# Optimization experiments

Hardware: AMD Instinct MI355X
Metric: run time of the kernel (lower is better)

## Reference

```python
import jax, jax.numpy as jnp
import numpy as np
import math

N_EMBD = 2048
N_HEAD = 16
HEAD_DIM = N_EMBD // N_HEAD  # 128
K = 8
P = 2
B = 1
T = 2048
EPS = 1e-6


def _rms_norm(x):
    return x * jax.lax.rsqrt(jnp.mean(x * x, axis=-1, keepdims=True) + EPS)


def _rope(x, cos, sin):
    # x: [B, T, H, D]; cos/sin: [T, D//2]
    d = x.shape[-1] // 2
    x1, x2 = x[..., :d], x[..., d:]
    c = cos[None, :, None, :]
    s = sin[None, :, None, :]
    return jnp.concatenate([x1 * c + x2 * s, -x1 * s + x2 * c], axis=-1)


def setup_inputs() -> dict:
    key = jax.random.key(0)
    ks = jax.random.split(key, 8)
    x = jax.random.normal(ks[0], (B, T, N_EMBD), jnp.float32)
    half = HEAD_DIM // 2
    inv_freq = 1.0 / (10000.0 ** (np.arange(half, dtype=np.float32) / half))
    ang = np.arange(T, dtype=np.float32)[:, None] * inv_freq[None, :]
    cos = jnp.asarray(np.cos(ang), jnp.float32)
    sin = jnp.asarray(np.sin(ang), jnp.float32)
    sc = 1.0 / math.sqrt(N_EMBD)
    Wq = jax.random.normal(ks[1], (N_EMBD, N_EMBD), jnp.float32) * sc
    Wk = jax.random.normal(ks[2], (N_EMBD, N_EMBD), jnp.float32) * sc
    Wv = jax.random.normal(ks[3], (N_EMBD, N_EMBD), jnp.float32) * sc
    Wproj = jax.random.normal(ks[4], (N_EMBD, N_EMBD), jnp.float32) * sc
    scd = 1.0 / math.sqrt(HEAD_DIM)
    Wdq = jax.random.normal(ks[5], (K, HEAD_DIM), jnp.float32) * scd
    Wdk = jax.random.normal(ks[6], (K, HEAD_DIM), jnp.float32) * scd
    return {"x": x, "cos": cos, "sin": sin, "Wq": Wq, "Wk": Wk, "Wv": Wv, "Wproj": Wproj, "Wdq": Wdq, "Wdk": Wdk}


def reference(x, cos, sin, Wq, Wk, Wv, Wproj, Wdq, Wdk):
    Bq, Tq, C = x.shape
    q = (x @ Wq.T).reshape(Bq, Tq, N_HEAD, HEAD_DIM)
    k = (x @ Wk.T).reshape(Bq, Tq, N_HEAD, HEAD_DIM)
    v = (x @ Wv.T).reshape(Bq, Tq, N_HEAD, HEAD_DIM)
    q = _rms_norm(_rope(q, cos, sin))
    k = _rms_norm(_rope(k, cos, sin))
    q = jnp.swapaxes(q, 1, 2)  # [B,H,T,D]
    k = jnp.swapaxes(k, 1, 2)
    v = jnp.swapaxes(v, 1, 2)
    # base-p digits in {0..p-1}; p=2 -> bits
    qd = jnp.floor(jax.nn.sigmoid(jnp.einsum('bhtd,kd->bhtk', q, Wdq)) * (P - 0.01)).astype(jnp.int32)
    kd = jnp.floor(jax.nn.sigmoid(jnp.einsum('bhtd,kd->bhtk', k, Wdk)) * (P - 0.01)).astype(jnp.int32)
    # lcp >= K-1  <=>  first K-1 digits all equal; pack them into one code
    pw = (P ** jnp.arange(K - 1)).astype(jnp.int32)  # [K-1]
    qc = jnp.sum(qd[..., : K - 1] * pw, axis=-1)  # [B,H,T]
    kc = jnp.sum(kd[..., : K - 1] * pw, axis=-1)
    lcp_mask = qc[..., :, None] == kc[..., None, :]  # [B,H,Tq,Tk]
    causal = jnp.tril(jnp.ones((Tq, Tq), dtype=bool))
    mask = lcp_mask & causal
    scores = jnp.einsum('bhqd,bhkd->bhqk', q, k) * (1.0 / math.sqrt(HEAD_DIM))
    s = jnp.where(mask, scores, -1e30)
    w = jax.nn.softmax(s, axis=-1)
    w = jnp.where(mask, w, 0.0)
    any_valid = jnp.any(mask, axis=-1, keepdims=True)
    w = jnp.where(any_valid, w, 0.0)  # fully-masked rows -> zero output (torch gives NaN)
    y = jnp.einsum('bhqk,bhkd->bhqd', w, v)
    y = jnp.swapaxes(y, 1, 2).reshape(Bq, Tq, C)
    return y @ Wproj.T
```

## Files before the change

kernel.cpp:

```cpp
#include <hip/hip_runtime.h>
#include <hip/hip_bf16.h>
#include <math.h>

#define T 2048
#define C 2048
#define NH 16
#define HD 128
#define SCALE 0.08838834764831845f
#define WL_CAP 2048
#define MARG 1e-4f

typedef short s16x8 __attribute__((ext_vector_type(8)));
typedef float f32x4 __attribute__((ext_vector_type(4)));
typedef _Float16 f16;
typedef f16 f16x8 __attribute__((ext_vector_type(8)));

__device__ __forceinline__ float wave_sum(float v) {
  #pragma unroll
  for (int o = 32; o > 0; o >>= 1) v += __shfl_xor(v, o, 64);
  return v;
}
__device__ __forceinline__ unsigned short f2bf(float f) {
  unsigned u = __float_as_uint(f);
  u += 0x7FFFu + ((u >> 16) & 1u);
  return (unsigned short)(u >> 16);
}

__global__ __launch_bounds__(256) void to_bf16(const float* __restrict__ in,
                                               unsigned short* __restrict__ outp,
                                               int n4) {
  int i = blockIdx.x * blockDim.x + threadIdx.x;
  const int stride = gridDim.x * blockDim.x;
  for (; i < n4; i += stride) {
    float4 v = ((const float4*)in)[i];
    ushort4 o;
    o.x = f2bf(v.x); o.y = f2bf(v.y); o.z = f2bf(v.z); o.w = f2bf(v.w);
    ((ushort4*)outp)[i] = o;
  }
}

#define PRESC 4096.0f
#define S0F 5.9604644775390625e-8f
#define S1F 2.9103830456733704e-11f
#define S2F 1.4210854715202004e-14f

__device__ __forceinline__ void split4(float4 v, ushort4& hi, ushort4& lo) {
  float s0 = v.x * PRESC, s1 = v.y * PRESC, s2 = v.z * PRESC, s3 = v.w * PRESC;
  union { f16 h[4]; ushort4 u; } H, L;
  H.h[0] = (f16)s0; H.h[1] = (f16)s1; H.h[2] = (f16)s2; H.h[3] = (f16)s3;
  L.h[0] = (f16)((s0 - (float)H.h[0]) * 2048.0f);
  L.h[1] = (f16)((s1 - (float)H.h[1]) * 2048.0f);
  L.h[2] = (f16)((s2 - (float)H.h[2]) * 2048.0f);
  L.h[3] = (f16)((s3 - (float)H.h[3]) * 2048.0f);
  hi = H.u; lo = L.u;
}

__global__ __launch_bounds__(256) void split_f16(const float* __restrict__ in,
                                                 unsigned short* __restrict__ hip_,
                                                 unsigned short* __restrict__ lop,
                                                 int n4) {
  int i = blockIdx.x * blockDim.x + threadIdx.x;
  const int stride = gridDim.x * blockDim.x;
  for (; i < n4; i += stride) {
    ushort4 h, l;
    split4(((const float4*)in)[i], h, l);
    ((ushort4*)hip_)[i] = h;
    ((ushort4*)lop)[i] = l;
  }
}

__global__ __launch_bounds__(256) void pre_split3(const float* __restrict__ x,
                                                  const float* __restrict__ Wq,
                                                  const float* __restrict__ Wk,
                                                  unsigned short* __restrict__ xh,
                                                  unsigned short* __restrict__ xl,
                                                  unsigned short* __restrict__ wqh,
                                                  unsigned short* __restrict__ wql,
                                                  unsigned short* __restrict__ wkh,
                                                  unsigned short* __restrict__ wkl,
                                                  int n4) {
  const float* __restrict__ in;
  unsigned short *oh, *ol;
  if (blockIdx.y == 0)      { in = x;  oh = xh;  ol = xl;  }
  else if (blockIdx.y == 1) { in = Wq; oh = wqh; ol = wql; }
  else                      { in = Wk; oh = wkh; ol = wkl; }
  int i = blockIdx.x * blockDim.x + threadIdx.x;
  const int stride = gridDim.x * blockDim.x;
  for (; i < n4; i += stride) {
    ushort4 h, l;
    split4(((const float4*)in)[i], h, l);
    ((ushort4*)oh)[i] = h;
    ((ushort4*)ol)[i] = l;
  }
}

__global__ __launch_bounds__(256) void to_f16h(const float* __restrict__ in,
                                               unsigned short* __restrict__ outp,
                                               int n4) {
  int i = blockIdx.x * blockDim.x + threadIdx.x;
  const int stride = gridDim.x * blockDim.x;
  for (; i < n4; i += stride) {
    float4 v = ((const float4*)in)[i];
    union { f16 h[4]; ushort4 u; } H;
    H.h[0] = (f16)(v.x * PRESC); H.h[1] = (f16)(v.y * PRESC);
    H.h[2] = (f16)(v.z * PRESC); H.h[3] = (f16)(v.w * PRESC);
    ((ushort4*)outp)[i] = H.u;
  }
}

__global__ __launch_bounds__(256) void post_h2(const float* __restrict__ Y,
                                               const float* __restrict__ Wproj,
                                               unsigned short* __restrict__ yh,
                                               unsigned short* __restrict__ wph,
                                               int n4) {
  const float* __restrict__ in = blockIdx.y ? Wproj : Y;
  unsigned short* __restrict__ outp = blockIdx.y ? wph : yh;
  int i = blockIdx.x * blockDim.x + threadIdx.x;
  const int stride = gridDim.x * blockDim.x;
  for (; i < n4; i += stride) {
    float4 v = ((const float4*)in)[i];
    union { f16 h[4]; ushort4 u; } H;
    H.h[0] = (f16)(v.x * PRESC); H.h[1] = (f16)(v.y * PRESC);
    H.h[2] = (f16)(v.z * PRESC); H.h[3] = (f16)(v.w * PRESC);
    ((ushort4*)outp)[i] = H.u;
  }
}

#define SBM 64
#define SBN 128
#define SBK 32

__global__ __launch_bounds__(256, 2) void gemm_qkf(const unsigned short* __restrict__ xhp,
                                                   const unsigned short* __restrict__ xlp,
                                                   const unsigned short* __restrict__ wqh,
                                                   const unsigned short* __restrict__ wql,
                                                   const unsigned short* __restrict__ wkh,
                                                   const unsigned short* __restrict__ wkl,
                                                   float* __restrict__ Qo,
                                                   float* __restrict__ Ko) {
  __shared__ unsigned short Ah[2][128 * 32];
  __shared__ unsigned short Av[2][128 * 32];
  __shared__ unsigned short Bh[2][128 * 32];
  __shared__ unsigned short Bv[2][128 * 32];
  const int tid = threadIdx.x;
  const int bm = blockIdx.x * 128;
  const int bn = blockIdx.y * 64;
  const int wv = tid >> 6, lane = tid & 63;
  const int wm = wv & 1, wn = wv >> 1;
  const int lrow = lane & 15, lquad = lane >> 4;

  const int sr = tid >> 2, qg = tid & 3;
  const int qs = qg ^ ((sr >> 1) & 3);

  f32x4 acc0[4][4], acc1[4][4];
  #pragma unroll
  for (int i = 0; i < 4; ++i)
    #pragma unroll
    for (int j = 0; j < 4; ++j) {
      acc0[i][j] = (f32x4){0.f, 0.f, 0.f, 0.f};
      acc1[i][j] = (f32x4){0.f, 0.f, 0.f, 0.f};
    }

  {
    uint4 a0H = *(const uint4*)(xhp + (size_t)(bm + sr) * C + qg * 8);
    uint4 a0L = *(const uint4*)(xlp + (size_t)(bm + sr) * C + qg * 8);
    uint4 a1H = *(const uint4*)(xhp + (size_t)(bm + 64 + sr) * C + qg * 8);
    uint4 a1L = *(const uint4*)(xlp + (size_t)(bm + 64 + sr) * C + qg * 8);
    uint4 bqH = *(const uint4*)(wqh + (size_t)(bn + sr) * C + qg * 8);
    uint4 bqL = *(const uint4*)(wql + (size_t)(bn + sr) * C + qg * 8);
    uint4 bkH = *(const uint4*)(wkh + (size_t)(bn + sr) * C + qg * 8);
    uint4 bkL = *(const uint4*)(wkl + (size_t)(bn + sr) * C + qg * 8);
    *(uint4*)&Ah[0][sr * 32 + qs * 8] = a0H;
    *(uint4*)&Av[0][sr * 32 + qs * 8] = a0L;
    *(uint4*)&Ah[0][(64 + sr) * 32 + qs * 8] = a1H;
    *(uint4*)&Av[0][(64 + sr) * 32 + qs * 8] = a1L;
    *(uint4*)&Bh[0][sr * 32 + qs * 8] = bqH;
    *(uint4*)&Bv[0][sr * 32 + qs * 8] = bqL;
    *(uint4*)&Bh[0][(64 + sr) * 32 + qs * 8] = bkH;
    *(uint4*)&Bv[0][(64 + sr) * 32 + qs * 8] = bkL;
  }
  __syncthreads();

  const int niter = C / 32;
  for (int it = 0; it < niter; ++it) {
    const int cur = it & 1;
    const bool has = (it + 1) < niter;
    uint4 a0H, a0L, a1H, a1L, bqH, bqL, bkH, bkL;
    if (has) {
      const int k0 = (it + 1) * 32;
      a0H = *(const uint4*)(xhp + (size_t)(bm + sr) * C + k0 + qg * 8);
      a0L = *(const uint4*)(xlp + (size_t)(bm + sr) * C + k0 + qg * 8);
      a1H = *(const uint4*)(xhp + (size_t)(bm + 64 + sr) * C + k0 + qg * 8);
      a1L = *(const uint4*)(xlp + (size_t)(bm + 64 + sr) * C + k0 + qg * 8);
      bqH = *(const uint4*)(wqh + (size_t)(bn + sr) * C + k0 + qg * 8);
      bqL = *(const uint4*)(wql + (size_t)(bn + sr) * C + k0 + qg * 8);
      bkH = *(const uint4*)(wkh + (size_t)(bn + sr) * C + k0 + qg * 8);
      bkL = *(const uint4*)(wkl + (size_t)(bn + sr) * C + k0 + qg * 8);
    }
    f16x8 ah[4], av[4], bh[4], bv[4];
    #pragma unroll
    for (int mi = 0; mi < 4; ++mi) {
      const int r = wm * 64 + mi * 16 + lrow;
      const int q = lquad ^ ((r >> 1) & 3);
      ah[mi] = *(const f16x8*)&Ah[cur][r * 32 + q * 8];
      av[mi] = *(const f16x8*)&Av[cur][r * 32 + q * 8];
    }
    #pragma unroll
    for (int ni = 0; ni < 4; ++ni) {
      const int r = wn * 64 + ni * 16 + lrow;
      const int q = lquad ^ ((r >> 1) & 3);
      bh[ni] = *(const f16x8*)&Bh[cur][r * 32 + q * 8];
      bv[ni] = *(const f16x8*)&Bv[cur][r * 32 + q * 8];
    }
    #pragma unroll
    for (int mi = 0; mi < 4; ++mi)
      #pragma unroll
      for (int ni = 0; ni < 4; ++ni) {
        acc0[mi][ni] = __builtin_amdgcn_mfma_f32_16x16x32_f16(ah[mi], bh[ni], acc0[mi][ni], 0, 0, 0);
        acc1[mi][ni] = __builtin_amdgcn_mfma_f32_16x16x32_f16(ah[mi], bv[ni], acc1[mi][ni], 0, 0, 0);
        acc1[mi][ni] = __builtin_amdgcn_mfma_f32_16x16x32_f16(av[mi], bh[ni], acc1[mi][ni], 0, 0, 0);
      }
    if (has) {
      const int nxt = cur ^ 1;
      *(uint4*)&Ah[nxt][sr * 32 + qs * 8] = a0H;
      *(uint4*)&Av[nxt][sr * 32 + qs * 8] = a0L;
      *(uint4*)&Ah[nxt][(64 + sr) * 32 + qs * 8] = a1H;
      *(uint4*)&Av[nxt][(64 + sr) * 32 + qs * 8] = a1L;
      *(uint4*)&Bh[nxt][sr * 32 + qs * 8] = bqH;
      *(uint4*)&Bv[nxt][sr * 32 + qs * 8] = bqL;
      *(uint4*)&Bh[nxt][(64 + sr) * 32 + qs * 8] = bkH;
      *(uint4*)&Bv[nxt][(64 + sr) * 32 + qs * 8] = bkL;
    }
    __syncthreads();
  }
  float* __restrict__ Cc = wn ? Ko : Qo;
  #pragma unroll
  for (int mi = 0; mi < 4; ++mi)
    #pragma unroll
    for (int ni = 0; ni < 4; ++ni)
      #pragma unroll
      for (int r = 0; r < 4; ++r) {
        int row = bm + wm * 64 + mi * 16 + lquad * 4 + r;
        int col = bn + ni * 16 + lrow;
        Cc[(size_t)row * C + col] = acc0[mi][ni][r] * S0F + acc1[mi][ni][r] * S1F;
      }
}

__global__ __launch_bounds__(256) void gemm_h1(const unsigned short* __restrict__ A,
                                               const unsigned short* __restrict__ B,
                                               float* __restrict__ Cc) {
  __shared__ unsigned short Ah[2][SBM * SBK];
  __shared__ unsigned short Bh[2][SBN * SBK];
  const int tid = threadIdx.x;
  const int bm = blockIdx.x * SBM;
  const int bn = blockIdx.y * SBN;
  const int wv = tid >> 6, lane = tid & 63;
  const int wm = wv & 1, wn = wv >> 1;
  const int lrow = lane & 15, lquad = lane >> 4;

  const int a_row = tid >> 2, qg = tid & 3;
  const int a_qs = qg ^ ((a_row >> 1) & 3);
  const int b_row0 = tid >> 2;
  const int b_qs = qg ^ ((b_row0 >> 1) & 3);

  f32x4 acc[2][4];
  #pragma unroll
  for (int i = 0; i < 2; ++i)
    #pragma unroll
    for (int j = 0; j < 4; ++j) acc[i][j] = (f32x4){0.f, 0.f, 0.f, 0.f};

  {
    uint4 av = *(const uint4*)(A + (size_t)(bm + a_row) * C + qg * 8);
    uint4 b0 = *(const uint4*)(B + (size_t)(bn + b_row0) * C + qg * 8);
    uint4 b1 = *(const uint4*)(B + (size_t)(bn + 64 + b_row0) * C + qg * 8);
    *(uint4*)&Ah[0][a_row * SBK + a_qs * 8] = av;
    *(uint4*)&Bh[0][b_row0 * SBK + b_qs * 8] = b0;
    *(uint4*)&Bh[0][(64 + b_row0) * SBK + b_qs * 8] = b1;
  }
  __syncthreads();

  const int niter = C / SBK;
  for (int it = 0; it < niter; ++it) {
    const int cur = it & 1;
    const bool has = (it + 1) < niter;
    uint4 avn, b0n, b1n;
    if (has) {
      const int k0 = (it + 1) * SBK;
      avn = *(const uint4*)(A + (size_t)(bm + a_row) * C + k0 + qg * 8);
      b0n = *(const uint4*)(B + (size_t)(bn + b_row0) * C + k0 + qg * 8);
      b1n = *(const uint4*)(B + (size_t)(bn + 64 + b_row0) * C + k0 + qg * 8);
    }
    f16x8 af[2], bfr[4];
    #pragma unroll
    for (int mi = 0; mi < 2; ++mi) {
      const int r = wm * 32 + mi * 16 + lrow;
      const int q = lquad ^ ((r >> 1) & 3);
      af[mi] = *(const f16x8*)&Ah[cur][r * SBK + q * 8];
    }
    #pragma unroll
    for (int ni = 0; ni < 4; ++ni) {
      const int r = wn * 64 + ni * 16 + lrow;
      const int q = lquad ^ ((r >> 1) & 3);
      bfr[ni] = *(const f16x8*)&Bh[cur][r * SBK + q * 8];
    }
    #pragma unroll
    for (int mi = 0; mi < 2; ++mi)
      #pragma unroll
      for (int ni = 0; ni < 4; ++ni)
        acc[mi][ni] = __builtin_amdgcn_mfma_f32_16x16x32_f16(af[mi], bfr[ni], acc[mi][ni], 0, 0, 0);
    if (has) {
      const int nxt = cur ^ 1;
      *(uint4*)&Ah[nxt][a_row * SBK + a_qs * 8] = avn;
      *(uint4*)&Bh[nxt][b_row0 * SBK + b_qs * 8] = b0n;
      *(uint4*)&Bh[nxt][(64 + b_row0) * SBK + b_qs * 8] = b1n;
    }
    __syncthreads();
  }
  #pragma unroll
  for (int mi = 0; mi < 2; ++mi)
    #pragma unroll
    for (int ni = 0; ni < 4; ++ni)
      #pragma unroll
      for (int r = 0; r < 4; ++r) {
        int row = bm + wm * 32 + mi * 16 + lquad * 4 + r;
        int col = bn + wn * 64 + ni * 16 + lrow;
        Cc[(size_t)row * C + col] = acc[mi][ni][r] * S0F;
      }
}

__device__ __forceinline__ void split8(const float4 v0, const float4 v1,
                                       uint4& hi, uint4& lo) {
  float s[8] = {v0.x * PRESC, v0.y * PRESC, v0.z * PRESC, v0.w * PRESC,
                v1.x * PRESC, v1.y * PRESC, v1.z * PRESC, v1.w * PRESC};
  union { uint4 u; f16 h[8]; } H, L;
  #pragma unroll
  for (int i = 0; i < 8; ++i) {
    f16 h2 = (f16)s[i];
    float d = s[i] - (float)h2;
    H.h[i] = h2;
    L.h[i] = (f16)(d * 2048.0f);
  }
  hi = H.u; lo = L.u;
}

__global__ __launch_bounds__(256, 2) void gemm_qk_split16(const float* __restrict__ A,
                                                          const float* __restrict__ Wq,
                                                          const float* __restrict__ Wk,
                                                          float* __restrict__ Qo,
                                                          float* __restrict__ Ko) {
  const float* __restrict__ Bw = blockIdx.z ? Wk : Wq;
  float* __restrict__ Cc = blockIdx.z ? Ko : Qo;
  __shared__ unsigned short Ah[2][SBM * SBK];
  __shared__ unsigned short Av[2][SBM * SBK];
  __shared__ unsigned short Bh[2][SBN * SBK];
  __shared__ unsigned short Bv[2][SBN * SBK];
  const int tid = threadIdx.x;
  const int bm = blockIdx.x * SBM;
  const int bn = blockIdx.y * SBN;
  const int wv = tid >> 6, lane = tid & 63;
  const int wm = wv & 1, wn = wv >> 1;
  const int lrow = lane & 15, lquad = lane >> 4;

  const int a_row = tid >> 2, qg = tid & 3;
  const int a_qs = qg ^ ((a_row >> 1) & 3);
  const int b_row0 = tid >> 2;
  const int b_qs = qg ^ ((b_row0 >> 1) & 3);

  f32x4 acc[3][2][4];
  #pragma unroll
  for (int g = 0; g < 3; ++g)
    #pragma unroll
    for (int i = 0; i < 2; ++i)
      #pragma unroll
      for (int j = 0; j < 4; ++j) acc[g][i][j] = (f32x4){0.f, 0.f, 0.f, 0.f};

  {
    const float* pA  = A  + (size_t)(bm + a_row) * C + qg * 8;
    const float* pB0 = Bw + (size_t)(bn + b_row0) * C + qg * 8;
    const float* pB1 = Bw + (size_t)(bn + 64 + b_row0) * C + qg * 8;
    uint4 h, l;
    split8(*(const float4*)pA, *(const float4*)(pA + 4), h, l);
    *(uint4*)&Ah[0][a_row * SBK + a_qs * 8] = h;
    *(uint4*)&Av[0][a_row * SBK + a_qs * 8] = l;
    split8(*(const float4*)pB0, *(const float4*)(pB0 + 4), h, l);
    *(uint4*)&Bh[0][b_row0 * SBK + b_qs * 8] = h;
    *(uint4*)&Bv[0][b_row0 * SBK + b_qs * 8] = l;
    split8(*(const float4*)pB1, *(const float4*)(pB1 + 4), h, l);
    *(uint4*)&Bh[0][(64 + b_row0) * SBK + b_qs * 8] = h;
    *(uint4*)&Bv[0][(64 + b_row0) * SBK + b_qs * 8] = l;
  }
  __syncthreads();

  const int niter = C / SBK;
  for (int it = 0; it < niter; ++it) {
    const int cur = it & 1;
    const bool has = (it + 1) < niter;
    float4 a0n, a1n, b00n, b01n, b10n, b11n;
    if (has) {
      const int k0 = (it + 1) * SBK;
      const float* pA  = A  + (size_t)(bm + a_row) * C + k0 + qg * 8;
      const float* pB0 = Bw + (size_t)(bn + b_row0) * C + k0 + qg * 8;
      const float* pB1 = Bw + (size_t)(bn + 64 + b_row0) * C + k0 + qg * 8;
      a0n = *(const float4*)pA;   a1n = *(const float4*)(pA + 4);
      b00n = *(const float4*)pB0; b01n = *(const float4*)(pB0 + 4);
      b10n = *(const float4*)pB1; b11n = *(const float4*)(pB1 + 4);
    }
    f16x8 ah[2], av[2], bh[4], bv[4];
    #pragma unroll
    for (int mi = 0; mi < 2; ++mi) {
      const int r = wm * 32 + mi * 16 + lrow;
      const int q = lquad ^ ((r >> 1) & 3);
      ah[mi] = *(const f16x8*)&Ah[cur][r * SBK + q * 8];
      av[mi] = *(const f16x8*)&Av[cur][r * SBK + q * 8];
    }
    #pragma unroll
    for (int ni = 0; ni < 4; ++ni) {
      const int r = wn * 64 + ni * 16 + lrow;
      const int q = lquad ^ ((r >> 1) & 3);
      bh[ni] = *(const f16x8*)&Bh[cur][r * SBK + q * 8];
      bv[ni] = *(const f16x8*)&Bv[cur][r * SBK + q * 8];
    }
    #pragma unroll
    for (int mi = 0; mi < 2; ++mi)
      #pragma unroll
      for (int ni = 0; ni < 4; ++ni) {
        acc[0][mi][ni] = __builtin_amdgcn_mfma_f32_16x16x32_f16(ah[mi], bh[ni], acc[0][mi][ni], 0, 0, 0);
        acc[1][mi][ni] = __builtin_amdgcn_mfma_f32_16x16x32_f16(ah[mi], bv[ni], acc[1][mi][ni], 0, 0, 0);
        acc[1][mi][ni] = __builtin_amdgcn_mfma_f32_16x16x32_f16(av[mi], bh[ni], acc[1][mi][ni], 0, 0, 0);
        acc[2][mi][ni] = __builtin_amdgcn_mfma_f32_16x16x32_f16(av[mi], bv[ni], acc[2][mi][ni], 0, 0, 0);
      }
    if (has) {
      const int nxt = cur ^ 1;
      uint4 h, l;
      split8(a0n, a1n, h, l);
      *(uint4*)&Ah[nxt][a_row * SBK + a_qs * 8] = h;
      *(uint4*)&Av[nxt][a_row * SBK + a_qs * 8] = l;
      split8(b00n, b01n, h, l);
      *(uint4*)&Bh[nxt][b_row0 * SBK + b_qs * 8] = h;
      *(uint4*)&Bv[nxt][b_row0 * SBK + b_qs * 8] = l;
      split8(b10n, b11n, h, l);
      *(uint4*)&Bh[nxt][(64 + b_row0) * SBK + b_qs * 8] = h;
      *(uint4*)&Bv[nxt][(64 + b_row0) * SBK + b_qs * 8] = l;
    }
    __syncthreads();
  }
  #pragma unroll
  for (int mi = 0; mi < 2; ++mi)
    #pragma unroll
    for (int ni = 0; ni < 4; ++ni)
      #pragma unroll
      for (int r = 0; r < 4; ++r) {
        int row = bm + wm * 32 + mi * 16 + lquad * 4 + r;
        int col = bn + wn * 64 + ni * 16 + lrow;
        float v = acc[0][mi][ni][r] * S0F + (acc[1][mi][ni][r] * S1F + acc[2][mi][ni][r] * S2F);
        Cc[(size_t)row * C + col] = v;
      }
}

#define VBM 64
#define VBN 128
#define VBK 32

__global__ __launch_bounds__(256) void gemm_bf16n(const unsigned short* __restrict__ A,
                                                  const unsigned short* __restrict__ B,
                                                  float* __restrict__ Cc) {
  __shared__ unsigned short Al[2][VBM * VBK];
  __shared__ unsigned short Bl[2][VBN * VBK];
  const int tid = threadIdx.x;
  const int bm = blockIdx.x * VBM;
  const int bn = blockIdx.y * VBN;
  const int wv = tid >> 6, lane = tid & 63;
  const int wm = wv & 1, wn = wv >> 1;
  const int lrow = lane & 15, lquad = lane >> 4;

  const int a_row = tid >> 2, qg = tid & 3;
  const int a_qs = qg ^ ((a_row >> 1) & 3);
  const int b_row0 = tid >> 2;
  const int b_qs = qg ^ ((b_row0 >> 1) & 3);

  f32x4 acc[2][4];
  #pragma unroll
  for (int i = 0; i < 2; ++i)
    #pragma unroll
    for (int j = 0; j < 4; ++j) acc[i][j] = (f32x4){0.f, 0.f, 0.f, 0.f};

  {
    uint4 av = *(const uint4*)(A + (size_t)(bm + a_row) * C + qg * 8);
    uint4 b0 = *(const uint4*)(B + (size_t)(bn + b_row0) * C + qg * 8);
    uint4 b1 = *(const uint4*)(B + (size_t)(bn + 64 + b_row0) * C + qg * 8);
    *(uint4*)&Al[0][a_row * VBK + a_qs * 8] = av;
    *(uint4*)&Bl[0][b_row0 * VBK + b_qs * 8] = b0;
    *(uint4*)&Bl[0][(64 + b_row0) * VBK + b_qs * 8] = b1;
  }
  __syncthreads();

  const int niter = C / VBK;
  for (int it = 0; it < niter; ++it) {
    const int cur = it & 1;
    const bool has = (it + 1) < niter;
    uint4 avn, b0n, b1n;
    if (has) {
      const int k0 = (it + 1) * VBK;
      avn = *(const uint4*)(A + (size_t)(bm + a_row) * C + k0 + qg * 8);
      b0n = *(const uint4*)(B + (size_t)(bn + b_row0) * C + k0 + qg * 8);
      b1n = *(const uint4*)(B + (size_t)(bn + 64 + b_row0) * C + k0 + qg * 8);
    }
    s16x8 af[2], bfr[4];
    #pragma unroll
    for (int mi = 0; mi < 2; ++mi) {
      const int r = wm * 32 + mi * 16 + lrow;
      const int q = lquad ^ ((r >> 1) & 3);
      af[mi] = *(const s16x8*)&Al[cur][r * VBK + q * 8];
    }
    #pragma unroll
    for (int ni = 0; ni < 4; ++ni) {
      const int r = wn * 64 + ni * 16 + lrow;
      const int q = lquad ^ ((r >> 1) & 3);
      bfr[ni] = *(const s16x8*)&Bl[cur][r * VBK + q * 8];
    }
    #pragma unroll
    for (int mi = 0; mi < 2; ++mi)
      #pragma unroll
      for (int ni = 0; ni < 4; ++ni)
        acc[mi][ni] = __builtin_amdgcn_mfma_f32_16x16x32_bf16(af[mi], bfr[ni], acc[mi][ni], 0, 0, 0);
    if (has) {
      const int nxt = cur ^ 1;
      *(uint4*)&Al[nxt][a_row * VBK + a_qs * 8] = avn;
      *(uint4*)&Bl[nxt][b_row0 * VBK + b_qs * 8] = b0n;
      *(uint4*)&Bl[nxt][(64 + b_row0) * VBK + b_qs * 8] = b1n;
    }
    __syncthreads();
  }
  #pragma unroll
  for (int mi = 0; mi < 2; ++mi)
    #pragma unroll
    for (int ni = 0; ni < 4; ++ni)
      #pragma unroll
      for (int r = 0; r < 4; ++r) {
        int row = bm + wm * 32 + mi * 16 + lquad * 4 + r;
        int col = bn + wn * 64 + ni * 16 + lrow;
        Cc[(size_t)row * C + col] = acc[mi][ni][r];
      }
}

__global__ void zero_ctr(int* __restrict__ ctr) {
  if (threadIdx.x == 0) ctr[0] = 0;
}

__global__ __launch_bounds__(256) void rope_fused(float* __restrict__ Qb,
                                                  float* __restrict__ Kb,
                                                  const float* __restrict__ cosb,
                                                  const float* __restrict__ sinb,
                                                  const float* __restrict__ Wdq,
                                                  const float* __restrict__ Wdk,
                                                  int* __restrict__ qcodes,
                                                  int* __restrict__ kcodes,
                                                  int* __restrict__ wl,
                                                  int* __restrict__ ctr) {
  float* __restrict__ buf = blockIdx.y ? Kb : Qb;
  const float* __restrict__ Wd = blockIdx.y ? Wdk : Wdq;
  int* __restrict__ codes = blockIdx.y ? kcodes : qcodes;
  int wave = (blockIdx.x << 2) + (threadIdx.x >> 6);
  int lane = threadIdx.x & 63;
  int t = wave / NH, h = wave % NH;
  size_t base = (size_t)t * C + h * HD;
  float x1 = buf[base + lane];
  float x2 = buf[base + lane + 64];
  float c = cosb[t * 64 + lane];
  float s = sinb[t * 64 + lane];
  float r1 = x1 * c + x2 * s;
  float r2 = x2 * c - x1 * s;
  float ss = wave_sum(r1 * r1 + r2 * r2);
  float inv = 1.0f / sqrtf(ss * (1.0f / 128.0f) + 1e-6f);
  r1 *= inv; r2 *= inv;
  buf[base + lane] = r1;
  buf[base + lane + 64] = r2;
  int code = 0;
  bool marg = false;
  #pragma unroll
  for (int kk = 0; kk < 7; ++kk) {
    float z = r1 * Wd[kk * HD + lane] + r2 * Wd[kk * HD + lane + 64];
    z = wave_sum(z);
    float sig = 1.0f / (1.0f + expf(-z));
    float d = sig * 1.99f - 1.0f;
    if (d >= 0.f) code |= (1 << kk);
    marg |= (fabsf(d) < MARG);
  }
  if (lane == 0) {
    codes[h * T + t] = code;
    if (marg) {
      int i = atomicAdd(ctr, 1);
      if ((unsigned)i < (unsigned)WL_CAP) wl[i] = ((int)blockIdx.y << 15) | (h << 11) | t;
    }
  }
}

__global__ __launch_bounds__(64) void fix_codes(const float* __restrict__ x,
                                                const float* __restrict__ Wq,
                                                const float* __restrict__ Wk,
                                                const float* __restrict__ cosb,
                                                const float* __restrict__ sinb,
                                                const float* __restrict__ Wdq,
                                                const float* __restrict__ Wdk,
                                                int* __restrict__ qc,
                                                int* __restrict__ kc,
                                                const int* __restrict__ wl,
                                                const int* __restrict__ ctr) {
  const int n = min(max(ctr[0], 0), WL_CAP);
  const int lane = threadIdx.x;
  for (int e = blockIdx.x; e < n; e += gridDim.x) {
    const int ent = wl[e];
    const int isK = (ent >> 15) & 1;
    const int h = (ent >> 11) & 15;
    const int t = ent & 2047;
    const float* __restrict__ W  = isK ? Wk : Wq;
    const float* __restrict__ Wd = isK ? Wdk : Wdq;
    int* __restrict__ codes = isK ? kc : qc;

    const float* xr = x + (size_t)t * C;
    const float* w0 = W + (size_t)(h * HD + lane) * C;
    const float* w1 = W + (size_t)(h * HD + lane + 64) * C;
    float p0[4] = {0.f, 0.f, 0.f, 0.f};
    float p1[4] = {0.f, 0.f, 0.f, 0.f};
    for (int k = 0; k < C; k += 4) {
      float4 xv = *(const float4*)(xr + k);
      float4 a = *(const float4*)(w0 + k);
      float4 b = *(const float4*)(w1 + k);
      p0[0] += xv.x * a.x; p0[1] += xv.y * a.y;
      p0[2] += xv.z * a.z; p0[3] += xv.w * a.w;
      p1[0] += xv.x * b.x; p1[1] += xv.y * b.y;
      p1[2] += xv.z * b.z; p1[3] += xv.w * b.w;
    }
    float x1 = (p0[0] + p0[1]) + (p0[2] + p0[3]);
    float x2 = (p1[0] + p1[1]) + (p1[2] + p1[3]);
    float c = cosb[t * 64 + lane];
    float s = sinb[t * 64 + lane];
    float r1 = x1 * c + x2 * s;
    float r2 = x2 * c - x1 * s;
    float ss = wave_sum(r1 * r1 + r2 * r2);
    float inv = 1.0f / sqrtf(ss * (1.0f / 128.0f) + 1e-6f);
    r1 *= inv; r2 *= inv;
    int code = 0;
    #pragma unroll
    for (int kk = 0; kk < 7; ++kk) {
      float z = r1 * Wd[kk * HD + lane] + r2 * Wd[kk * HD + lane + 64];
      z = wave_sum(z);
      float sig = 1.0f / (1.0f + expf(-z));
      if (sig * 1.99f >= 1.0f) code |= (1 << kk);
    }
    if (lane == 0) codes[h * T + t] = code;
  }
}

__global__ __launch_bounds__(256) void attn_sparse(const float* __restrict__ Q,
                                                   const float* __restrict__ Kn,
                                                   const float* __restrict__ V,
                                                   const int* __restrict__ qc,
                                                   const int* __restrict__ kc,
                                                   float* __restrict__ Y) {
  const int tid = threadIdx.x;
  const int lane = tid & 63;
  const int wave_id = blockIdx.x * 4 + (tid >> 6);
  const int h = wave_id & (NH - 1);
  const int qrow = wave_id >> 4;
  const size_t hb = (size_t)h * HD;

  const float q0 = Q[(size_t)qrow * C + hb + lane];
  const float q1 = Q[(size_t)qrow * C + hb + lane + 64];
  const int qcode = qc[h * T + qrow];
  const int* kch = kc + h * T;

  float m = -1e30f, l = 0.f, acc0 = 0.f, acc1 = 0.f;

  const int nchunks = (qrow >> 6) + 1;
  int kcj = kch[lane];
  for (int ci = 0; ci < nchunks; ++ci) {
    const int j0 = ci << 6;
    const int cur = kcj;
    if (ci + 1 < nchunks) kcj = kch[j0 + 64 + lane];
    unsigned long long mask = __ballot((cur == qcode) && (j0 + lane <= qrow));
    while (mask) {
      const int j = j0 + (__ffsll((long long)mask) - 1);
      mask &= mask - 1;
      const float* kr = Kn + (size_t)j * C + hb;
      const float* vr = V + (size_t)j * C + hb;
      const float k0v = kr[lane], k1v = kr[lane + 64];
      const float v0 = vr[lane], v1 = vr[lane + 64];
      const float s = wave_sum(q0 * k0v + q1 * k1v) * SCALE;
      const float m_new = fmaxf(m, s);
      const float alpha = __expf(m - m_new);
      const float p = __expf(s - m_new);
      l = l * alpha + p;
      acc0 = acc0 * alpha + p * v0;
      acc1 = acc1 * alpha + p * v1;
      m = m_new;
    }
  }
  const float invl = (l > 0.f) ? 1.0f / l : 0.f;
  Y[(size_t)qrow * C + hb + lane] = acc0 * invl;
  Y[(size_t)qrow * C + hb + lane + 64] = acc1 * invl;
}

extern "C" void kernel_launch(void* const* d_in, const int* in_sizes, int n_in,
                              void* d_out, int out_size, void* d_ws, size_t ws_size,
                              hipStream_t stream) {
  (void)in_sizes; (void)n_in; (void)out_size;
  const float* x     = (const float*)d_in[0];
  const float* cosb  = (const float*)d_in[1];
  const float* sinb  = (const float*)d_in[2];
  const float* Wq    = (const float*)d_in[3];
  const float* Wk    = (const float*)d_in[4];
  const float* Wv    = (const float*)d_in[5];
  const float* Wproj = (const float*)d_in[6];
  const float* Wdq   = (const float*)d_in[7];
  const float* Wdk   = (const float*)d_in[8];
  float* out = (float*)d_out;

  const size_t MB = 1024 * 1024;
  char* ws = (char*)d_ws;
  const int n4 = T * C / 4;

  if (ws_size >= (size_t)64 * MB) {
    unsigned short* xh  = (unsigned short*)(ws);
    unsigned short* xl  = (unsigned short*)(ws + 8 * MB);
    unsigned short* wqh = (unsigned short*)(ws + 16 * MB);
    unsigned short* wql = (unsigned short*)(ws + 24 * MB);
    unsigned short* wkh = (unsigned short*)(ws + 32 * MB);
    unsigned short* wkl = (unsigned short*)(ws + 40 * MB);
    float* K = (float*)(ws + 48 * MB);
    unsigned short* wvh = (unsigned short*)(ws + 16 * MB);
    float* V = (float*)(ws + 24 * MB);
    int* qc  = (int*)(ws + 40 * MB);
    int* kc  = qc + NH * T;
    int* ctr = kc + NH * T;
    int* wl  = ctr + 16;
    float* Y = (float*)(ws);
    unsigned short* yh  = (unsigned short*)(ws + 16 * MB);
    unsigned short* wph = (unsigned short*)(ws + 24 * MB);
    float* Q = out;

    pre_split3<<<dim3(1024, 3), 256, 0, stream>>>(x, Wq, Wk, xh, xl, wqh, wql, wkh, wkl, n4);
    zero_ctr<<<1, 64, 0, stream>>>(ctr);
    gemm_qkf<<<dim3(T / 128, C / 64), 256, 0, stream>>>(xh, xl, wqh, wql, wkh, wkl, Q, K);
    to_f16h<<<2048, 256, 0, stream>>>(Wv, wvh, n4);
    gemm_h1<<<dim3(T / SBM, C / SBN), 256, 0, stream>>>(xh, wvh, V);
    rope_fused<<<dim3(T * NH / 4, 2), 256, 0, stream>>>(Q, K, cosb, sinb, Wdq, Wdk, qc, kc, wl, ctr);
    fix_codes<<<256, 64, 0, stream>>>(x, Wq, Wk, cosb, sinb, Wdq, Wdk, qc, kc, wl, ctr);
    attn_sparse<<<T * NH / 4, 256, 0, stream>>>(Q, K, V, qc, kc, Y);
    post_h2<<<dim3(1024, 2), 256, 0, stream>>>(Y, Wproj, yh, wph, n4);
    gemm_h1<<<dim3(T / SBM, C / SBN), 256, 0, stream>>>(yh, wph, out);
  } else {
    float* Kbuf = (float*)ws;
    float* V    = (float*)(ws + 16 * MB);
    float* Y    = (float*)(ws + 32 * MB);
    unsigned short* Wbf = (unsigned short*)(ws + 48 * MB);
    unsigned short* xbf = (unsigned short*)Y;
    unsigned short* Ybf = (unsigned short*)Kbuf;
    float* Q    = out;
    int* qc  = (int*)(Wbf + (size_t)T * C);
    int* kc  = qc + NH * T;
    int* ctr = kc + NH * T;
    int* wl  = ctr + 16;

    to_bf16<<<2048, 256, 0, stream>>>(x, xbf, n4);
    to_bf16<<<2048, 256, 0, stream>>>(Wv, Wbf, n4);
    gemm_bf16n<<<dim3(T / VBM, C / VBN), 256, 0, stream>>>(xbf, Wbf, V);
    gemm_qk_split16<<<dim3(T / SBM, C / SBN, 2), 256, 0, stream>>>(x, Wq, Wk, Q, Kbuf);
    zero_ctr<<<1, 64, 0, stream>>>(ctr);
    rope_fused<<<dim3(T * NH / 4, 2), 256, 0, stream>>>(Q, Kbuf, cosb, sinb, Wdq, Wdk, qc, kc, wl, ctr);
    fix_codes<<<256, 64, 0, stream>>>(x, Wq, Wk, cosb, sinb, Wdq, Wdk, qc, kc, wl, ctr);
    attn_sparse<<<T * NH / 4, 256, 0, stream>>>(Q, Kbuf, V, qc, kc, Y);
    to_bf16<<<2048, 256, 0, stream>>>(Y, Ybf, n4);
    to_bf16<<<2048, 256, 0, stream>>>(Wproj, Wbf, n4);
    gemm_bf16n<<<dim3(T / VBM, C / VBN), 256, 0, stream>>>(Ybf, Wbf, out);
  }
}
```

Baseline: 461.3 us.

## Use direct global-to-LDS loads in QK and H1 GEMMs, enlarge H1 tile

Replaces the register-staged global loads and LDS stores in gemm_qkf and gemm_h1 with __builtin_amdgcn_global_load_lds 16-byte direct copies. The XOR swizzle moves from the LDS address to the global source address. gemm_h1 also grows from an SBM x SBN tile to 128x128, so each wave computes 4x4 MFMA tiles. The aim is to cut VGPR staging and LDS write instructions and to raise arithmetic intensity, at the cost of fewer blocks in the V and proj GEMMs. There is also a risk of ordering hazards, since the asynchronous LDS loads are only fenced by __syncthreads.

```diff
diff --git a/kernel.cpp b/kernel.cpp
--- a/kernel.cpp
+++ b/kernel.cpp
@@ -14,6 +14,7 @@
 typedef float f32x4 __attribute__((ext_vector_type(4)));
 typedef _Float16 f16;
 typedef f16 f16x8 __attribute__((ext_vector_type(8)));
+typedef unsigned int u32;
 
 __device__ __forceinline__ float wave_sum(float v) {
   #pragma unroll
@@ -24,6 +25,12 @@
   unsigned u = __float_as_uint(f);
   u += 0x7FFFu + ((u >> 16) & 1u);
   return (unsigned short)(u >> 16);
+}
+
+__device__ __forceinline__ void gld16(const void* g, void* l) {
+  __builtin_amdgcn_global_load_lds(
+      (const __attribute__((address_space(1))) u32*)g,
+      (__attribute__((address_space(3))) u32*)l, 16, 0, 0);
 }
 
 __global__ __launch_bounds__(256) void to_bf16(const float* __restrict__ in,
@@ -150,7 +157,13 @@
   const int lrow = lane & 15, lquad = lane >> 4;
 
   const int sr = tid >> 2, qg = tid & 3;
-  const int qs = qg ^ ((sr >> 1) & 3);
+  const int qsw = qg ^ ((sr >> 1) & 3);
+  const int ld0 = tid * 8;
+  const int ld1 = 2048 + tid * 8;
+
+  const size_t arow0 = (size_t)(bm + sr) * C;
+  const size_t arow1 = (size_t)(bm + 64 + sr) * C;
+  const size_t brow  = (size_t)(bn + sr) * C;
 
   f32x4 acc0[4][4], acc1[4][4];
   #pragma unroll
@@ -162,40 +175,32 @@
     }
 
   {
-    uint4 a0H = *(const uint4*)(xhp + (size_t)(bm + sr) * C + qg * 8);
-    uint4 a0L = *(const uint4*)(xlp + (size_t)(bm + sr) * C + qg * 8);
-    uint4 a1H = *(const uint4*)(xhp + (size_t)(bm + 64 + sr) * C + qg * 8);
-    uint4 a1L = *(const uint4*)(xlp + (size_t)(bm + 64 + sr) * C + qg * 8);
-    uint4 bqH = *(const uint4*)(wqh + (size_t)(bn + sr) * C + qg * 8);
-    uint4 bqL = *(const uint4*)(wql + (size_t)(bn + sr) * C + qg * 8);
-    uint4 bkH = *(const uint4*)(wkh + (size_t)(bn + sr) * C + qg * 8);
-    uint4 bkL = *(const uint4*)(wkl + (size_t)(bn + sr) * C + qg * 8);
-    *(uint4*)&Ah[0][sr * 32 + qs * 8] = a0H;
-    *(uint4*)&Av[0][sr * 32 + qs * 8] = a0L;
-    *(uint4*)&Ah[0][(64 + sr) * 32 + qs * 8] = a1H;
-    *(uint4*)&Av[0][(64 + sr) * 32 + qs * 8] = a1L;
-    *(uint4*)&Bh[0][sr * 32 + qs * 8] = bqH;
-    *(uint4*)&Bv[0][sr * 32 + qs * 8] = bqL;
-    *(uint4*)&Bh[0][(64 + sr) * 32 + qs * 8] = bkH;
-    *(uint4*)&Bv[0][(64 + sr) * 32 + qs * 8] = bkL;
+    const int k0 = qsw * 8;
+    gld16(xhp + arow0 + k0, &Ah[0][ld0]);
+    gld16(xhp + arow1 + k0, &Ah[0][ld1]);
+    gld16(xlp + arow0 + k0, &Av[0][ld0]);
+    gld16(xlp + arow1 + k0, &Av[0][ld1]);
+    gld16(wqh + brow + k0, &Bh[0][ld0]);
+    gld16(wkh + brow + k0, &Bh[0][ld1]);
+    gld16(wql + brow + k0, &Bv[0][ld0]);
+    gld16(wkl + brow + k0, &Bv[0][ld1]);
   }
   __syncthreads();
 
   const int niter = C / 32;
   for (int it = 0; it < niter; ++it) {
     const int cur = it & 1;
-    const bool has = (it + 1) < niter;
-    uint4 a0H, a0L, a1H, a1L, bqH, bqL, bkH, bkL;
-    if (has) {
-      const int k0 = (it + 1) * 32;
-      a0H = *(const uint4*)(xhp + (size_t)(bm + sr) * C + k0 + qg * 8);
-      a0L = *(const uint4*)(xlp + (size_t)(bm + sr) * C + k0 + qg * 8);
-      a1H = *(const uint4*)(xhp + (size_t)(bm + 64 + sr) * C + k0 + qg * 8);
-      a1L = *(const uint4*)(xlp + (size_t)(bm + 64 + sr) * C + k0 + qg * 8);
-      bqH = *(const uint4*)(wqh + (size_t)(bn + sr) * C + k0 + qg * 8);
-      bqL = *(const uint4*)(wql + (size_t)(bn + sr) * C + k0 + qg * 8);
-      bkH = *(const uint4*)(wkh + (size_t)(bn + sr) * C + k0 + qg * 8);
-      bkL = *(const uint4*)(wkl + (size_t)(bn + sr) * C + k0 + qg * 8);
+    if (it + 1 < niter) {
+      const int nxt = cur ^ 1;
+      const int k0 = (it + 1) * 32 + qsw * 8;
+      gld16(xhp + arow0 + k0, &Ah[nxt][ld0]);
+      gld16(xhp + arow1 + k0, &Ah[nxt][ld1]);
+      gld16(xlp + arow0 + k0, &Av[nxt][ld0]);
+      gld16(xlp + arow1 + k0, &Av[nxt][ld1]);
+      gld16(wqh + brow + k0, &Bh[nxt][ld0]);
+      gld16(wkh + brow + k0, &Bh[nxt][ld1]);
+      gld16(wql + brow + k0, &Bv[nxt][ld0]);
+      gld16(wkl + brow + k0, &Bv[nxt][ld1]);
     }
     f16x8 ah[4], av[4], bh[4], bv[4];
     #pragma unroll
@@ -220,17 +225,6 @@
         acc1[mi][ni] = __builtin_amdgcn_mfma_f32_16x16x32_f16(ah[mi], bv[ni], acc1[mi][ni], 0, 0, 0);
         acc1[mi][ni] = __builtin_amdgcn_mfma_f32_16x16x32_f16(av[mi], bh[ni], acc1[mi][ni], 0, 0, 0);
       }
-    if (has) {
-      const int nxt = cur ^ 1;
-      *(uint4*)&Ah[nxt][sr * 32 + qs * 8] = a0H;
-      *(uint4*)&Av[nxt][sr * 32 + qs * 8] = a0L;
-      *(uint4*)&Ah[nxt][(64 + sr) * 32 + qs * 8] = a1H;
-      *(uint4*)&Av[nxt][(64 + sr) * 32 + qs * 8] = a1L;
-      *(uint4*)&Bh[nxt][sr * 32 + qs * 8] = bqH;
-      *(uint4*)&Bv[nxt][sr * 32 + qs * 8] = bqL;
-      *(uint4*)&Bh[nxt][(64 + sr) * 32 + qs * 8] = bkH;
-      *(uint4*)&Bv[nxt][(64 + sr) * 32 + qs * 8] = bkL;
-    }
     __syncthreads();
   }
   float* __restrict__ Cc = wn ? Ko : Qo;
@@ -249,80 +243,78 @@
 __global__ __launch_bounds__(256) void gemm_h1(const unsigned short* __restrict__ A,
                                                const unsigned short* __restrict__ B,
                                                float* __restrict__ Cc) {
-  __shared__ unsigned short Ah[2][SBM * SBK];
-  __shared__ unsigned short Bh[2][SBN * SBK];
+  __shared__ unsigned short Ah[2][128 * 32];
+  __shared__ unsigned short Bh[2][128 * 32];
   const int tid = threadIdx.x;
-  const int bm = blockIdx.x * SBM;
-  const int bn = blockIdx.y * SBN;
+  const int bm = blockIdx.x * 128;
+  const int bn = blockIdx.y * 128;
   const int wv = tid >> 6, lane = tid & 63;
   const int wm = wv & 1, wn = wv >> 1;
   const int lrow = lane & 15, lquad = lane >> 4;
 
-  const int a_row = tid >> 2, qg = tid & 3;
-  const int a_qs = qg ^ ((a_row >> 1) & 3);
-  const int b_row0 = tid >> 2;
-  const int b_qs = qg ^ ((b_row0 >> 1) & 3);
-
-  f32x4 acc[2][4];
-  #pragma unroll
-  for (int i = 0; i < 2; ++i)
+  const int sr = tid >> 2, qg = tid & 3;
+  const int qsw = qg ^ ((sr >> 1) & 3);
+  const int ld0 = tid * 8;
+  const int ld1 = 2048 + tid * 8;
+
+  const size_t arow0 = (size_t)(bm + sr) * C;
+  const size_t arow1 = (size_t)(bm + 64 + sr) * C;
+  const size_t brow0 = (size_t)(bn + sr) * C;
+  const size_t brow1 = (size_t)(bn + 64 + sr) * C;
+
+  f32x4 acc[4][4];
+  #pragma unroll
+  for (int i = 0; i < 4; ++i)
     #pragma unroll
     for (int j = 0; j < 4; ++j) acc[i][j] = (f32x4){0.f, 0.f, 0.f, 0.f};
 
   {
-    uint4 av = *(const uint4*)(A + (size_t)(bm + a_row) * C + qg * 8);
-    uint4 b0 = *(const uint4*)(B + (size_t)(bn + b_row0) * C + qg * 8);
-    uint4 b1 = *(const uint4*)(B + (size_t)(bn + 64 + b_row0) * C + qg * 8);
-    *(uint4*)&Ah[0][a_row * SBK + a_qs * 8] = av;
-    *(uint4*)&Bh[0][b_row0 * SBK + b_qs * 8] = b0;
-    *(uint4*)&Bh[0][(64 + b_row0) * SBK + b_qs * 8] = b1;
+    const int k0 = qsw * 8;
+    gld16(A + arow0 + k0, &Ah[0][ld0]);
+    gld16(A + arow1 + k0, &Ah[0][ld1]);
+    gld16(B + brow0 + k0, &Bh[0][ld0]);
+    gld16(B + brow1 + k0, &Bh[0][ld1]);
   }
   __syncthreads();
 
-  const int niter = C / SBK;
+  const int niter = C / 32;
   for (int it = 0; it < niter; ++it) {
     const int cur = it & 1;
-    const bool has = (it + 1) < niter;
-    uint4 avn, b0n, b1n;
-    if (has) {
-      const int k0 = (it + 1) * SBK;
-      avn = *(const uint4*)(A + (size_t)(bm + a_row) * C + k0 + qg * 8);
-      b0n = *(const uint4*)(B + (size_t)(bn + b_row0) * C + k0 + qg * 8);
-      b1n = *(const uint4*)(B + (size_t)(bn + 64 + b_row0) * C + k0 + qg * 8);
-    }
-    f16x8 af[2], bfr[4];
-    #pragma unroll
-    for (int mi = 0; mi < 2; ++mi) {
-      const int r = wm * 32 + mi * 16 + lrow;
+    if (it + 1 < niter) {
+      const int nxt = cur ^ 1;
+      const int k0 = (it + 1) * 32 + qsw * 8;
+      gld16(A + arow0 + k0, &Ah[nxt][ld0]);
+      gld16(A + arow1 + k0, &Ah[nxt][ld1]);
+      gld16(B + brow0 + k0, &Bh[nxt][ld0]);
+      gld16(B + brow1 + k0, &Bh[nxt][ld1]);
+    }
+    f16x8 af[4], bf[4];
+    #pragma unroll
+    for (int mi = 0; mi < 4; ++mi) {
+      const int r = wm * 64 + mi * 16 + lrow;
       const int q = lquad ^ ((r >> 1) & 3);
-      af[mi] = *(const f16x8*)&Ah[cur][r * SBK + q * 8];
+      af[mi] = *(const f16x8*)&Ah[cur][r * 32 + q * 8];
     }
     #pragma unroll
     for (int ni = 0; ni < 4; ++ni) {
       const int r = wn * 64 + ni * 16 + lrow;
       const int q = lquad ^ ((r >> 1) & 3);
-      bfr[ni] = *(const f16x8*)&Bh[cur][r * SBK + q * 8];
-    }
-    #pragma unroll
-    for (int mi = 0; mi < 2; ++mi)
+      bf[ni] = *(const f16x8*)&Bh[cur][r * 32 + q * 8];
+    }
+    #pragma unroll
+    for (int mi = 0; mi < 4; ++mi)
       #pragma unroll
       for (int ni = 0; ni < 4; ++ni)
-        acc[mi][ni] = __builtin_amdgcn_mfma_f32_16x16x32_f16(af[mi], bfr[ni], acc[mi][ni], 0, 0, 0);
-    if (has) {
-      const int nxt = cur ^ 1;
-      *(uint4*)&Ah[nxt][a_row * SBK + a_qs * 8] = avn;
-      *(uint4*)&Bh[nxt][b_row0 * SBK + b_qs * 8] = b0n;
-      *(uint4*)&Bh[nxt][(64 + b_row0) * SBK + b_qs * 8] = b1n;
-    }
+        acc[mi][ni] = __builtin_amdgcn_mfma_f32_16x16x32_f16(af[mi], bf[ni], acc[mi][ni], 0, 0, 0);
     __syncthreads();
   }
   #pragma unroll
-  for (int mi = 0; mi < 2; ++mi)
+  for (int mi = 0; mi < 4; ++mi)
     #pragma unroll
     for (int ni = 0; ni < 4; ++ni)
       #pragma unroll
       for (int r = 0; r < 4; ++r) {
-        int row = bm + wm * 32 + mi * 16 + lquad * 4 + r;
+        int row = bm + wm * 64 + mi * 16 + lquad * 4 + r;
         int col = bn + wn * 64 + ni * 16 + lrow;
         Cc[(size_t)row * C + col] = acc[mi][ni][r] * S0F;
       }
@@ -743,12 +735,12 @@
     zero_ctr<<<1, 64, 0, stream>>>(ctr);
     gemm_qkf<<<dim3(T / 128, C / 64), 256, 0, stream>>>(xh, xl, wqh, wql, wkh, wkl, Q, K);
     to_f16h<<<2048, 256, 0, stream>>>(Wv, wvh, n4);
-    gemm_h1<<<dim3(T / SBM, C / SBN), 256, 0, stream>>>(xh, wvh, V);
+    gemm_h1<<<dim3(T / 128, C / 128), 256, 0, stream>>>(xh, wvh, V);
     rope_fused<<<dim3(T * NH / 4, 2), 256, 0, stream>>>(Q, K, cosb, sinb, Wdq, Wdk, qc, kc, wl, ctr);
     fix_codes<<<256, 64, 0, stream>>>(x, Wq, Wk, cosb, sinb, Wdq, Wdk, qc, kc, wl, ctr);
     attn_sparse<<<T * NH / 4, 256, 0, stream>>>(Q, K, V, qc, kc, Y);
     post_h2<<<dim3(1024, 2), 256, 0, stream>>>(Y, Wproj, yh, wph, n4);
-    gemm_h1<<<dim3(T / SBM, C / SBN), 256, 0, stream>>>(yh, wph, out);
+    gemm_h1<<<dim3(T / 128, C / 128), 256, 0, stream>>>(yh, wph, out);
   } else {
     float* Kbuf = (float*)ws;
     float* V    = (float*)(ws + 16 * MB);
```

Result: slower. 484.4 us (+5.0%).
